# Performance work log

Hardware: AMD Instinct MI355X
Metric: run time of the kernel (lower is better)

The kernel has to match this reference:

```python
import jax, jax.numpy as jnp
import numpy as np


def _lin_interp(x, out_size):
    # x: [..., T_in]; matches torch F.interpolate(mode='linear', align_corners=False)
    t_in = x.shape[-1]
    scale = t_in / out_size
    pos = (jnp.arange(out_size, dtype=jnp.float32) + 0.5) * scale - 0.5
    pos = jnp.clip(pos, 0.0, t_in - 1)
    lo = jnp.floor(pos).astype(jnp.int32)
    hi = jnp.minimum(lo + 1, t_in - 1)
    w = (pos - lo.astype(jnp.float32)).astype(x.dtype)
    return x[..., lo] * (1.0 - w) + x[..., hi] * w


def _lin_init(k, fan_in, shape):
    lim = 1.0 / np.sqrt(fan_in)
    return jax.random.uniform(k, shape, jnp.float32, -lim, lim)


def setup_inputs() -> dict:
    key = jax.random.key(0)
    ks = jax.random.split(key, 32)
    B, T, NMEL = 8, 1024, 80
    TV, H, W = 32, 112, 112
    S = 4  # max_speakers
    d = {}
    d['audio_input'] = jax.random.normal(ks[0], (B, T, NMEL), jnp.float32)
    d['video_input'] = jax.random.normal(ks[1], (B, TV, 3, H, W), jnp.float32)
    d['w_ae'] = _lin_init(ks[2], 80, (80, 256)); d['b_ae'] = _lin_init(ks[3], 80, (256,))
    d['ln_g'] = jnp.ones((256,), jnp.float32); d['ln_b'] = jnp.zeros((256,), jnp.float32)
    d['w_a1'] = _lin_init(ks[4], 256, (256, 512)); d['b_a1'] = _lin_init(ks[5], 256, (512,))
    d['w_a2'] = _lin_init(ks[6], 512, (512, 256)); d['b_a2'] = _lin_init(ks[7], 512, (256,))
    fan = 3 * 7 * 7
    d['conv_w'] = _lin_init(ks[8], fan, (64, 3, 7, 7)); d['conv_b'] = _lin_init(ks[9], fan, (64,))
    d['w_vfc'] = _lin_init(ks[10], 64, (64, 256)); d['b_vfc'] = _lin_init(ks[11], 64, (256,))
    d['w_f1'] = _lin_init(ks[12], 512, (512, 512)); d['b_f1'] = _lin_init(ks[13], 512, (512,))
    d['w_f2'] = _lin_init(ks[14], 512, (512, 256)); d['b_f2'] = _lin_init(ks[15], 512, (256,))
    d['heads_w'] = _lin_init(ks[16], 256, (S, 256, 80)); d['heads_b'] = _lin_init(ks[17], 256, (S, 80))
    d['w_spk'] = _lin_init(ks[18], 256, (256, S)); d['b_spk'] = _lin_init(ks[19], 256, (S,))
    return d


def reference(audio_input, video_input, w_ae, b_ae, ln_g, ln_b, w_a1, b_a1, w_a2, b_a2,
              conv_w, conv_b, w_vfc, b_vfc, w_f1, b_f1, w_f2, b_f2,
              heads_w, heads_b, w_spk, b_spk):
    # ---- audio branch ----
    a = audio_input @ w_ae + b_ae                      # [B,T,256]
    mu = a.mean(-1, keepdims=True)
    var = a.var(-1, keepdims=True)
    a = (a - mu) * jax.lax.rsqrt(var + 1e-5) * ln_g + ln_b
    a = jax.nn.relu(a @ w_a1 + b_a1) @ w_a2 + b_a2     # dropout is identity at eval
    # ---- video branch ----
    B, TV, C, H, W = video_input.shape
    v = video_input.reshape(B * TV, C, H, W)
    v = jax.lax.conv_general_dilated(v, conv_w, (2, 2), [(3, 3), (3, 3)],
                                     dimension_numbers=('NCHW', 'OIHW', 'NCHW'))
    v = v + conv_b[None, :, None, None]
    v = v.mean((2, 3))                                  # AdaptiveAvgPool2d((1,1))
    v = (v @ w_vfc + b_vfc).reshape(B, TV, 256)
    T = a.shape[1]
    if TV != T:
        v = _lin_interp(v.transpose(0, 2, 1), T).transpose(0, 2, 1)  # [B,T,256]
    # ---- fusion ----
    f = jnp.concatenate([a, v], axis=-1)                # [B,T,512]
    f = jax.nn.relu(f @ w_f1 + b_f1) @ w_f2 + b_f2      # [B,T,256]
    # ---- per-speaker heads as one batched GEMM ----
    specs = jnp.einsum('btd,sdo->bsto', f, heads_w) + heads_b[None, :, None, :]  # [B,S,T,80]
    # ---- specs -> waveforms (vectorized over batch x speakers) ----
    S = specs.shape[1]
    wave_len = T * 160  # samples_per_frame = 160
    noise = jax.random.normal(jax.random.key(1234), (B, S, wave_len), jnp.float32) * 0.1
    energy = _lin_interp(specs.sum(-1), wave_len)       # [B,S,wave_len]
    waveforms = noise * (energy * 0.5 + 0.5)
    # ---- speaker classifier ----
    speaker_logits = f.mean(1) @ w_spk + b_spk          # [B,S]
    return waveforms, specs, speaker_logits
```

## Files before the change

### kernel.cpp

```cpp
#include <hip/hip_runtime.h>
#include <hip/hip_bf16.h>
#include <math.h>

typedef _Float16 f16;
typedef f16 f16x8 __attribute__((ext_vector_type(8)));
typedef f16 f16x4 __attribute__((ext_vector_type(4)));
typedef float f32x4 __attribute__((ext_vector_type(4)));

template<int RELU, int OUT>
__global__ __launch_bounds__(256) void hgemm(
    const f16* __restrict__ A, const f16* __restrict__ Wt,
    const float* __restrict__ bias,
    void* __restrict__ Cout, int ldc, int col_off,
    int N, int K, float* __restrict__ colsum)
{
  __shared__ f16 As[128 * 64];
  __shared__ f16 Bs[64 * 64];
  const int tid = threadIdx.x;
  const int wave = tid >> 6, lane = tid & 63;
  const int wm = (wave >> 1) * 64;
  const int wn = (wave & 1) * 32;
  const int m0 = blockIdx.y * 128;
  const int n0 = blockIdx.x * 64;
  const int q = lane >> 4, r16 = lane & 15;

  f32x4 acc[4][2];
#pragma unroll
  for (int mi = 0; mi < 4; mi++)
#pragma unroll
    for (int ni = 0; ni < 2; ni++) acc[mi][ni] = (f32x4)0.f;

  for (int k0 = 0; k0 < K; k0 += 64) {
    f16x8 areg[4], breg[2];
#pragma unroll
    for (int i = 0; i < 4; i++) {
      const int G = i * 256 + tid, row = G >> 3, g = G & 7;
      areg[i] = *(const f16x8*)(A + (size_t)(m0 + row) * K + k0 + g * 8);
    }
#pragma unroll
    for (int i = 0; i < 2; i++) {
      const int G = i * 256 + tid, row = G >> 3, g = G & 7;
      breg[i] = *(const f16x8*)(Wt + (size_t)(n0 + row) * K + k0 + g * 8);
    }
#pragma unroll
    for (int i = 0; i < 4; i++) {
      const int G = i * 256 + tid, row = G >> 3, g = G & 7;
      *(f16x8*)((char*)As + row * 128 + ((g ^ (row & 7)) * 16)) = areg[i];
    }
#pragma unroll
    for (int i = 0; i < 2; i++) {
      const int G = i * 256 + tid, row = G >> 3, g = G & 7;
      *(f16x8*)((char*)Bs + row * 128 + ((g ^ (row & 7)) * 16)) = breg[i];
    }
    __syncthreads();
#pragma unroll
    for (int h = 0; h < 2; h++) {
      const int kg = h * 4 + q;
      f16x8 af[4], bf[2];
#pragma unroll
      for (int mi = 0; mi < 4; mi++) {
        const int row = wm + mi * 16 + r16;
        af[mi] = *(const f16x8*)((char*)As + row * 128 + ((kg ^ (row & 7)) * 16));
      }
#pragma unroll
      for (int ni = 0; ni < 2; ni++) {
        const int row = wn + ni * 16 + r16;
        bf[ni] = *(const f16x8*)((char*)Bs + row * 128 + ((kg ^ (row & 7)) * 16));
      }
#pragma unroll
      for (int mi = 0; mi < 4; mi++)
#pragma unroll
        for (int ni = 0; ni < 2; ni++)
          acc[mi][ni] = __builtin_amdgcn_mfma_f32_16x16x32_f16(
              af[mi], bf[ni], acc[mi][ni], 0, 0, 0);
    }
    __syncthreads();
  }

#pragma unroll
  for (int ni = 0; ni < 2; ni++) {
    const int n = n0 + wn + ni * 16 + r16;
    const float bv = bias[n];
    const int s_ = n / 80, o_ = n - s_ * 80;
    float csum = 0.f;
#pragma unroll
    for (int mi = 0; mi < 4; mi++) {
#pragma unroll
      for (int rr = 0; rr < 4; rr++) {
        const int m = m0 + wm + mi * 16 + q * 4 + rr;
        float v = acc[mi][ni][rr] + bv;
        if (RELU) v = fmaxf(v, 0.f);
        if (OUT == 2) csum += v;
        if (OUT == 0)
          ((float*)Cout)[(size_t)m * ldc + col_off + n] = v;
        else if (OUT == 3) {
          const int b_ = m >> 10, t_ = m & 1023;
          ((float*)Cout)[((size_t)((b_ * 4 + s_) * 1024 + t_)) * 80 + o_] = v;
        } else
          ((f16*)Cout)[(size_t)m * ldc + col_off + n] = (f16)v;
      }
    }
    if (OUT == 2) {
      csum += __shfl_xor(csum, 16);
      csum += __shfl_xor(csum, 32);
      if (q == 0) atomicAdd(&colsum[(m0 >> 10) * 256 + n], csum);
    }
  }
}

__global__ __launch_bounds__(256) void prep_kernel(
    const float* __restrict__ audio,
    const float* __restrict__ w_ae, const float* __restrict__ w_a1,
    const float* __restrict__ w_a2, const float* __restrict__ w_f1,
    const float* __restrict__ w_f2, const float* __restrict__ heads_w,
    const float* __restrict__ heads_b,
    f16* __restrict__ a_h, f16* __restrict__ wae_t, f16* __restrict__ wa1_t,
    f16* __restrict__ wa2_t, f16* __restrict__ wf1_t, f16* __restrict__ wf2_t,
    f16* __restrict__ wh_t, float* __restrict__ bp, float* __restrict__ colsum)
{
  int idx = blockIdx.x * 256 + threadIdx.x;
  if (idx < 1048576) {
    const int row = idx >> 7, col = idx & 127;
    a_h[idx] = (f16)(col < 80 ? audio[(size_t)row * 80 + col] : 0.f);
    return;
  }
  idx -= 1048576;
  if (idx < 32768) {
    const int n = idx >> 7, k = idx & 127;
    wae_t[idx] = (f16)(k < 80 ? w_ae[k * 256 + n] : 0.f);
    return;
  }
  idx -= 32768;
  if (idx < 131072) { const int n = idx >> 8, k = idx & 255; wa1_t[idx] = (f16)w_a1[k * 512 + n]; return; }
  idx -= 131072;
  if (idx < 131072) { const int n = idx >> 9, k = idx & 511; wa2_t[idx] = (f16)w_a2[k * 256 + n]; return; }
  idx -= 131072;
  if (idx < 262144) { const int n = idx >> 9, k = idx & 511; wf1_t[idx] = (f16)w_f1[k * 512 + n]; return; }
  idx -= 262144;
  if (idx < 131072) { const int n = idx >> 9, k = idx & 511; wf2_t[idx] = (f16)w_f2[k * 256 + n]; return; }
  idx -= 131072;
  if (idx < 81920) {
    const int n = idx >> 8, d = idx & 255;
    const int s = n / 80, o = n - s * 80;
    wh_t[idx] = (f16)heads_w[(size_t)(s * 256 + d) * 80 + o];
    return;
  }
  idx -= 81920;
  if (idx < 320) { bp[idx] = heads_b[idx]; return; }
  idx -= 320;
  if (idx < 2048) colsum[idx] = 0.f;
}

__global__ __launch_bounds__(256) void layernorm_f16(
    const float* __restrict__ a, const float* __restrict__ g,
    const float* __restrict__ b, f16* __restrict__ out)
{
  const int row = blockIdx.x * 4 + (threadIdx.x >> 6);
  const int lane = threadIdx.x & 63;
  const float4 v = ((const float4*)(a + (size_t)row * 256))[lane];
  float s = v.x + v.y + v.z + v.w;
#pragma unroll
  for (int off = 32; off > 0; off >>= 1) s += __shfl_down(s, off);
  const float mu = __shfl(s, 0) * (1.0f / 256.0f);
  const float dx = v.x - mu, dy = v.y - mu, dz = v.z - mu, dw = v.w - mu;
  float s2 = dx * dx + dy * dy + dz * dz + dw * dw;
#pragma unroll
  for (int off = 32; off > 0; off >>= 1) s2 += __shfl_down(s2, off);
  const float var = __shfl(s2, 0) * (1.0f / 256.0f);
  const float r = rsqrtf(var + 1e-5f);
  const float4 gg = ((const float4*)g)[lane];
  const float4 bb = ((const float4*)b)[lane];
  f16x4 o;
  o[0] = (f16)(dx * r * gg.x + bb.x);
  o[1] = (f16)(dy * r * gg.y + bb.y);
  o[2] = (f16)(dz * r * gg.z + bb.z);
  o[3] = (f16)(dw * r * gg.w + bb.w);
  ((f16x4*)(out + (size_t)row * 256))[lane] = o;
}

__global__ __launch_bounds__(256) void video_reduce_kernel(
    const float* __restrict__ x, float* __restrict__ Sg)
{
  const int img = blockIdx.x;
  const float* p = x + (size_t)img * 12544;
  __shared__ float rowS[2][112];
  __shared__ float c0s[112], c1s[112], c109s[112], c110s[112], c111s[112];
  __shared__ float base[14];
  __shared__ float sE[7], sO[7];
  const int t = threadIdx.x;
  if (t < 224) {
    const int r = t >> 1;
    const int par = t & 1;
    const float* rp = p + r * 112 + par;
    float s = 0.f;
#pragma unroll
    for (int i = 0; i < 56; i++) s += rp[2 * i];
    rowS[par][r] = s;
    if (par == 0) { c0s[r] = rp[0]; c110s[r] = rp[110]; }
    else { c1s[r] = rp[0]; c109s[r] = rp[108]; c111s[r] = rp[110]; }
  }
  __syncthreads();
  if (t < 14) {
    const int arr = t >> 1;
    const int rp = t & 1;
    const float* src = (arr == 0) ? rowS[0] : (arr == 1) ? rowS[1] :
                       (arr == 2) ? c0s : (arr == 3) ? c1s :
                       (arr == 4) ? c109s : (arr == 5) ? c110s : c111s;
    float s = 0.f;
    for (int r = rp; r < 112; r += 2) s += src[r];
    base[t] = s;
  }
  __syncthreads();
  if (t < 7) {
    float se, so;
    switch (t) {
      case 0: se = base[2] - base[8] - base[12]; so = base[3] - base[9] - base[13]; break;
      case 1: se = base[0] - base[10];           so = base[1] - base[11];           break;
      case 2: se = base[2] - base[12];           so = base[3] - base[13];           break;
      case 3: se = base[0];                      so = base[1];                      break;
      case 4: se = base[2];                      so = base[3];                      break;
      case 5: se = base[0] - base[4];            so = base[1] - base[5];            break;
      default: se = base[2] - base[6];           so = base[3] - base[7];            break;
    }
    sE[t] = se; sO[t] = so;
  }
  __syncthreads();
  if (t < 49) {
    const int kh = t / 7, kw = t % 7;
    auto ccol = [&](int r) -> float {
      switch (kw) {
        case 0: return rowS[1][r] - c109s[r] - c111s[r];
        case 1: return rowS[0][r] - c110s[r];
        case 2: return rowS[1][r] - c111s[r];
        case 3: return rowS[0][r];
        case 4: return rowS[1][r];
        case 5: return rowS[0][r] - c0s[r];
        default: return rowS[1][r] - c1s[r];
      }
    };
    float v;
    switch (kh) {
      case 0: v = sO[kw] - ccol(109) - ccol(111); break;
      case 1: v = sE[kw] - ccol(110);             break;
      case 2: v = sO[kw] - ccol(111);             break;
      case 3: v = sE[kw];                         break;
      case 4: v = sO[kw];                         break;
      case 5: v = sE[kw] - ccol(0);               break;
      default: v = sO[kw] - ccol(1);              break;
    }
    Sg[(size_t)img * 49 + t] = v;
  }
}

__global__ __launch_bounds__(256) void vpool_fc_kernel(
    const float* __restrict__ Sg, const float* __restrict__ conv_w,
    const float* __restrict__ conv_b, const float* __restrict__ w_vfc,
    const float* __restrict__ b_vfc, float* __restrict__ v256)
{
  __shared__ float vp[64];
  const int n = blockIdx.x, t = threadIdx.x;
  if (t < 64) {
    float acc = 0.f;
    const float* s = Sg + (size_t)n * 147;
#pragma unroll 7
    for (int k = 0; k < 147; k++) acc = fmaf(conv_w[t * 147 + k], s[k], acc);
    vp[t] = conv_b[t] + acc * (1.0f / 3136.0f);
  }
  __syncthreads();
  float acc = 0.f;
#pragma unroll
  for (int k = 0; k < 64; k++) acc = fmaf(vp[k], w_vfc[k * 256 + t], acc);
  v256[(size_t)n * 256 + t] = acc + b_vfc[t];
}

__global__ __launch_bounds__(256) void interp_video_f16(
    const float* __restrict__ v256, f16* __restrict__ fbuf)
{
  const int idx = blockIdx.x * 256 + threadIdx.x;
  const int c = idx & 255;
  const int t = (idx >> 8) & 1023;
  const int b = idx >> 18;
  float pos = ((float)t + 0.5f) * 0.03125f - 0.5f;
  pos = fminf(fmaxf(pos, 0.0f), 31.0f);
  const int lo = (int)floorf(pos);
  int hi = lo + 1; if (hi > 31) hi = 31;
  const float w = pos - (float)lo;
  const float vl = v256[(size_t)(b * 32 + lo) * 256 + c];
  const float vh = v256[(size_t)(b * 32 + hi) * 256 + c];
  fbuf[(size_t)(b * 1024 + t) * 512 + 256 + c] = (f16)(vl * (1.0f - w) + vh * w);
}

__global__ __launch_bounds__(256) void energy_kernel(
    const float* __restrict__ specs, float* __restrict__ energy)
{
  const int row = blockIdx.x * 256 + threadIdx.x;
  const float4* src = (const float4*)(specs + (size_t)row * 80);
  float sum = 0.f;
#pragma unroll
  for (int i = 0; i < 20; i++) {
    const float4 v = src[i];
    sum += v.x + v.y + v.z + v.w;
  }
  energy[row] = sum;
}

__device__ __forceinline__ unsigned rotl32(unsigned x, int d) {
  return (x << d) | (x >> (32 - d));
}

__device__ __forceinline__ float erfinv_xla(float x) {
  float w = -log1pf(-x * x);
  float p;
  if (w < 5.0f) {
    w = w - 2.5f;
    p = 2.81022636e-08f;
    p = fmaf(p, w, 3.43273939e-07f);
    p = fmaf(p, w, -3.5233877e-06f);
    p = fmaf(p, w, -4.39150654e-06f);
    p = fmaf(p, w, 0.00021858087f);
    p = fmaf(p, w, -0.00125372503f);
    p = fmaf(p, w, -0.00417768164f);
    p = fmaf(p, w, 0.246640727f);
    p = fmaf(p, w, 1.50140941f);
  } else {
    w = sqrtf(w) - 3.0f;
    p = -0.000200214257f;
    p = fmaf(p, w, 0.000100950558f);
    p = fmaf(p, w, 0.00134934322f);
    p = fmaf(p, w, -0.00367342844f);
    p = fmaf(p, w, 0.00573950773f);
    p = fmaf(p, w, -0.0076224613f);
    p = fmaf(p, w, 0.00943887047f);
    p = fmaf(p, w, 1.00167406f);
    p = fmaf(p, w, 2.83297682f);
  }
  return p * x;
}

__global__ __launch_bounds__(256) void waveform_kernel(
    const float* __restrict__ energy, float* __restrict__ out)
{
  const unsigned n = blockIdx.x * 256 + threadIdx.x;
  const unsigned ks0 = 0u, ks1 = 1234u;
  const unsigned ks2 = 0x1BD11BDAu ^ ks0 ^ ks1;
  unsigned x0 = ks0;
  unsigned x1 = n + ks1;
#define TF_R4(a, b, c, d)                        \
  x0 += x1; x1 = rotl32(x1, a); x1 ^= x0;        \
  x0 += x1; x1 = rotl32(x1, b); x1 ^= x0;        \
  x0 += x1; x1 = rotl32(x1, c); x1 ^= x0;        \
  x0 += x1; x1 = rotl32(x1, d); x1 ^= x0;
  TF_R4(13, 15, 26, 6)  x0 += ks1; x1 += ks2 + 1u;
  TF_R4(17, 29, 16, 24) x0 += ks2; x1 += ks0 + 2u;
  TF_R4(13, 15, 26, 6)  x0 += ks0; x1 += ks1 + 3u;
  TF_R4(17, 29, 16, 24) x0 += ks1; x1 += ks2 + 4u;
  TF_R4(13, 15, 26, 6)  x0 += ks2; x1 += ks0 + 5u;
#undef TF_R4
  const unsigned bits = x0 ^ x1;
  const float f = __uint_as_float((bits >> 9) | 0x3f800000u) - 1.0f;
  const float minv = -0.99999994f;
  const float u = fmaxf(minv, fmaf(f, 2.0f, minv));
  const float noise = 1.41421354f * erfinv_xla(u) * 0.1f;
  const unsigned i = n % 163840u;
  const unsigned bs = n / 163840u;
  float pos = ((float)i + 0.5f) * 0.00625f - 0.5f;
  pos = fminf(fmaxf(pos, 0.0f), 1023.0f);
  const int lo = (int)floorf(pos);
  int hi = lo + 1; if (hi > 1023) hi = 1023;
  const float w = pos - (float)lo;
  const float* e = energy + (size_t)bs * 1024;
  const float ev = e[lo] * (1.0f - w) + e[hi] * w;
  out[n] = noise * fmaf(ev, 0.5f, 0.5f);
}

__global__ __launch_bounds__(64) void spk_final_kernel(
    const float* __restrict__ colsum, const float* __restrict__ w_spk,
    const float* __restrict__ b_spk, float* __restrict__ out)
{
  const int idx = threadIdx.x;
  if (idx < 32) {
    const int b = idx >> 2, s = idx & 3;
    const float* cs = colsum + b * 256;
    float acc = 0.f;
#pragma unroll 8
    for (int d = 0; d < 256; d++)
      acc = fmaf(cs[d] * (1.0f / 1024.0f), w_spk[d * 4 + s], acc);
    out[b * 4 + s] = acc + b_spk[s];
  }
}

extern "C" void kernel_launch(void* const* d_in, const int* in_sizes, int n_in,
                              void* d_out, int out_size, void* d_ws, size_t ws_size,
                              hipStream_t stream)
{
  (void)in_sizes; (void)n_in; (void)out_size; (void)ws_size;
  const float* audio   = (const float*)d_in[0];
  const float* video   = (const float*)d_in[1];
  const float* w_ae    = (const float*)d_in[2];
  const float* b_ae    = (const float*)d_in[3];
  const float* ln_g    = (const float*)d_in[4];
  const float* ln_b    = (const float*)d_in[5];
  const float* w_a1    = (const float*)d_in[6];
  const float* b_a1    = (const float*)d_in[7];
  const float* w_a2    = (const float*)d_in[8];
  const float* b_a2    = (const float*)d_in[9];
  const float* conv_w  = (const float*)d_in[10];
  const float* conv_b  = (const float*)d_in[11];
  const float* w_vfc   = (const float*)d_in[12];
  const float* b_vfc   = (const float*)d_in[13];
  const float* w_f1    = (const float*)d_in[14];
  const float* b_f1    = (const float*)d_in[15];
  const float* w_f2    = (const float*)d_in[16];
  const float* b_f2    = (const float*)d_in[17];
  const float* heads_w = (const float*)d_in[18];
  const float* heads_b = (const float*)d_in[19];
  const float* w_spk   = (const float*)d_in[20];
  const float* b_spk   = (const float*)d_in[21];

  float* ws = (float*)d_ws;
  float* a0     = ws;
  float* colsum = ws + 2097152;
  float* Sg     = ws + 2099200;
  float* v256   = ws + 2136832;
  float* energy = ws + 2202368;
  float* bp     = ws + 2235136;
  f16* fh = (f16*)(ws + 2235456);
  f16* a1     = fh;
  f16* h16    = a1 + 2097152;
  f16* fbuf16 = h16 + 4194304;
  f16* a_h    = fbuf16 + 4194304;
  f16* wae_t  = a_h + 1048576;
  f16* wa1_t  = wae_t + 32768;
  f16* wa2_t  = wa1_t + 131072;
  f16* wf1_t  = wa2_t + 131072;
  f16* wf2_t  = wf1_t + 262144;
  f16* wh_t   = wf2_t + 131072;

  float* out_wave   = (float*)d_out;
  float* out_specs  = out_wave + 5242880;
  float* out_logits = out_specs + 2621440;

  prep_kernel<<<7114, 256, 0, stream>>>(audio, w_ae, w_a1, w_a2, w_f1, w_f2,
                                        heads_w, heads_b,
                                        a_h, wae_t, wa1_t, wa2_t, wf1_t, wf2_t,
                                        wh_t, bp, colsum);

  video_reduce_kernel<<<768, 256, 0, stream>>>(video, Sg);
  vpool_fc_kernel<<<256, 256, 0, stream>>>(Sg, conv_w, conv_b, w_vfc, b_vfc, v256);

  hgemm<0, 0><<<dim3(4, 64), 256, 0, stream>>>(a_h, wae_t, b_ae, a0, 256, 0, 256, 128, nullptr);
  layernorm_f16<<<2048, 256, 0, stream>>>(a0, ln_g, ln_b, a1);
  hgemm<1, 1><<<dim3(8, 64), 256, 0, stream>>>(a1, wa1_t, b_a1, h16, 512, 0, 512, 256, nullptr);
  hgemm<0, 1><<<dim3(4, 64), 256, 0, stream>>>(h16, wa2_t, b_a2, fbuf16, 512, 0, 256, 512, nullptr);
  interp_video_f16<<<8192, 256, 0, stream>>>(v256, fbuf16);

  hgemm<1, 1><<<dim3(8, 64), 256, 0, stream>>>(fbuf16, wf1_t, b_f1, h16, 512, 0, 512, 512, nullptr);
  hgemm<0, 2><<<dim3(4, 64), 256, 0, stream>>>(h16, wf2_t, b_f2, a1, 256, 0, 256, 512, colsum);

  hgemm<0, 3><<<dim3(5, 64), 256, 0, stream>>>(a1, wh_t, bp, out_specs, 0, 0, 320, 256, nullptr);
  energy_kernel<<<128, 256, 0, stream>>>(out_specs, energy);

  waveform_kernel<<<20480, 256, 0, stream>>>(energy, out_wave);

  spk_final_kernel<<<1, 64, 0, stream>>>(colsum, w_spk, b_spk, out_logits);
}
```

Baseline: 263.8 us.

## Halve GEMM M-tile and double-buffer LDS with register prefetch

The hgemm kernel's M tile shrinks from 128 to 64 rows, which doubles the grid size for each GEMM launch. Shared-memory tiles are double-buffered and the next K slice is prefetched into registers while the current one is computed, so one of the two barriers per iteration goes away. The goal is better occupancy and overlap of global loads with MFMA work on these small GEMMs (M=8192). The cost is less data reuse per block, since B tiles are reloaded twice as often, and more blocks to schedule.

```diff
diff --git a/kernel.cpp b/kernel.cpp
--- a/kernel.cpp
+++ b/kernel.cpp
@@ -14,67 +14,76 @@
     void* __restrict__ Cout, int ldc, int col_off,
     int N, int K, float* __restrict__ colsum)
 {
-  __shared__ f16 As[128 * 64];
-  __shared__ f16 Bs[64 * 64];
+  __shared__ f16 As[2][64 * 64];
+  __shared__ f16 Bs[2][64 * 64];
   const int tid = threadIdx.x;
   const int wave = tid >> 6, lane = tid & 63;
-  const int wm = (wave >> 1) * 64;
+  const int wm = (wave >> 1) * 32;
   const int wn = (wave & 1) * 32;
-  const int m0 = blockIdx.y * 128;
+  const int m0 = blockIdx.y * 64;
   const int n0 = blockIdx.x * 64;
   const int q = lane >> 4, r16 = lane & 15;
 
-  f32x4 acc[4][2];
-#pragma unroll
-  for (int mi = 0; mi < 4; mi++)
+  const int c0 = tid, c1 = tid + 256;
+  const int rA0 = c0 >> 3, gA0 = c0 & 7;
+  const int rA1 = c1 >> 3, gA1 = c1 & 7;
+
+  const f16* pA0 = A + (size_t)(m0 + rA0) * K + gA0 * 8;
+  const f16* pA1 = A + (size_t)(m0 + rA1) * K + gA1 * 8;
+  const f16* pB0 = Wt + (size_t)(n0 + rA0) * K + gA0 * 8;
+  const f16* pB1 = Wt + (size_t)(n0 + rA1) * K + gA1 * 8;
+
+  const int sA0 = rA0 * 128 + ((gA0 ^ (rA0 & 7)) * 16);
+  const int sA1 = rA1 * 128 + ((gA1 ^ (rA1 & 7)) * 16);
+
+  f32x4 acc[2][2];
+#pragma unroll
+  for (int mi = 0; mi < 2; mi++)
 #pragma unroll
     for (int ni = 0; ni < 2; ni++) acc[mi][ni] = (f32x4)0.f;
 
-  for (int k0 = 0; k0 < K; k0 += 64) {
-    f16x8 areg[4], breg[2];
-#pragma unroll
-    for (int i = 0; i < 4; i++) {
-      const int G = i * 256 + tid, row = G >> 3, g = G & 7;
-      areg[i] = *(const f16x8*)(A + (size_t)(m0 + row) * K + k0 + g * 8);
-    }
-#pragma unroll
-    for (int i = 0; i < 2; i++) {
-      const int G = i * 256 + tid, row = G >> 3, g = G & 7;
-      breg[i] = *(const f16x8*)(Wt + (size_t)(n0 + row) * K + k0 + g * 8);
-    }
-#pragma unroll
-    for (int i = 0; i < 4; i++) {
-      const int G = i * 256 + tid, row = G >> 3, g = G & 7;
-      *(f16x8*)((char*)As + row * 128 + ((g ^ (row & 7)) * 16)) = areg[i];
-    }
-#pragma unroll
-    for (int i = 0; i < 2; i++) {
-      const int G = i * 256 + tid, row = G >> 3, g = G & 7;
-      *(f16x8*)((char*)Bs + row * 128 + ((g ^ (row & 7)) * 16)) = breg[i];
+  f16x8 ar0 = *(const f16x8*)pA0;
+  f16x8 ar1 = *(const f16x8*)pA1;
+  f16x8 br0 = *(const f16x8*)pB0;
+  f16x8 br1 = *(const f16x8*)pB1;
+
+  const int iters = K >> 6;
+  int p = 0;
+  for (int it = 0; it < iters; it++) {
+    *(f16x8*)((char*)As[p] + sA0) = ar0;
+    *(f16x8*)((char*)As[p] + sA1) = ar1;
+    *(f16x8*)((char*)Bs[p] + sA0) = br0;
+    *(f16x8*)((char*)Bs[p] + sA1) = br1;
+    if (it + 1 < iters) {
+      const int ko = (it + 1) << 6;
+      ar0 = *(const f16x8*)(pA0 + ko);
+      ar1 = *(const f16x8*)(pA1 + ko);
+      br0 = *(const f16x8*)(pB0 + ko);
+      br1 = *(const f16x8*)(pB1 + ko);
     }
     __syncthreads();
 #pragma unroll
     for (int h = 0; h < 2; h++) {
       const int kg = h * 4 + q;
-      f16x8 af[4], bf[2];
-#pragma unroll
-      for (int mi = 0; mi < 4; mi++) {
+      f16x8 af[2], bf[2];
+#pragma unroll
+      for (int mi = 0; mi < 2; mi++) {
         const int row = wm + mi * 16 + r16;
-        af[mi] = *(const f16x8*)((char*)As + row * 128 + ((kg ^ (row & 7)) * 16));
+        af[mi] = *(const f16x8*)((char*)As[p] + row * 128 + ((kg ^ (row & 7)) * 16));
       }
 #pragma unroll
       for (int ni = 0; ni < 2; ni++) {
         const int row = wn + ni * 16 + r16;
-        bf[ni] = *(const f16x8*)((char*)Bs + row * 128 + ((kg ^ (row & 7)) * 16));
+        bf[ni] = *(const f16x8*)((char*)Bs[p] + row * 128 + ((kg ^ (row & 7)) * 16));
       }
 #pragma unroll
-      for (int mi = 0; mi < 4; mi++)
+      for (int mi = 0; mi < 2; mi++)
 #pragma unroll
         for (int ni = 0; ni < 2; ni++)
           acc[mi][ni] = __builtin_amdgcn_mfma_f32_16x16x32_f16(
               af[mi], bf[ni], acc[mi][ni], 0, 0, 0);
     }
-    __syncthreads();
+    p ^= 1;
   }
 
 #pragma unroll
@@ -84,7 +93,7 @@
     const int s_ = n / 80, o_ = n - s_ * 80;
     float csum = 0.f;
 #pragma unroll
-    for (int mi = 0; mi < 4; mi++) {
+    for (int mi = 0; mi < 2; mi++) {
 #pragma unroll
       for (int rr = 0; rr < 4; rr++) {
         const int m = m0 + wm + mi * 16 + q * 4 + rr;
@@ -448,16 +457,16 @@
   video_reduce_kernel<<<768, 256, 0, stream>>>(video, Sg);
   vpool_fc_kernel<<<256, 256, 0, stream>>>(Sg, conv_w, conv_b, w_vfc, b_vfc, v256);
 
-  hgemm<0, 0><<<dim3(4, 64), 256, 0, stream>>>(a_h, wae_t, b_ae, a0, 256, 0, 256, 128, nullptr);
+  hgemm<0, 0><<<dim3(4, 128), 256, 0, stream>>>(a_h, wae_t, b_ae, a0, 256, 0, 256, 128, nullptr);
   layernorm_f16<<<2048, 256, 0, stream>>>(a0, ln_g, ln_b, a1);
-  hgemm<1, 1><<<dim3(8, 64), 256, 0, stream>>>(a1, wa1_t, b_a1, h16, 512, 0, 512, 256, nullptr);
-  hgemm<0, 1><<<dim3(4, 64), 256, 0, stream>>>(h16, wa2_t, b_a2, fbuf16, 512, 0, 256, 512, nullptr);
+  hgemm<1, 1><<<dim3(8, 128), 256, 0, stream>>>(a1, wa1_t, b_a1, h16, 512, 0, 512, 256, nullptr);
+  hgemm<0, 1><<<dim3(4, 128), 256, 0, stream>>>(h16, wa2_t, b_a2, fbuf16, 512, 0, 256, 512, nullptr);
   interp_video_f16<<<8192, 256, 0, stream>>>(v256, fbuf16);
 
-  hgemm<1, 1><<<dim3(8, 64), 256, 0, stream>>>(fbuf16, wf1_t, b_f1, h16, 512, 0, 512, 512, nullptr);
-  hgemm<0, 2><<<dim3(4, 64), 256, 0, stream>>>(h16, wf2_t, b_f2, a1, 256, 0, 256, 512, colsum);
-
-  hgemm<0, 3><<<dim3(5, 64), 256, 0, stream>>>(a1, wh_t, bp, out_specs, 0, 0, 320, 256, nullptr);
+  hgemm<1, 1><<<dim3(8, 128), 256, 0, stream>>>(fbuf16, wf1_t, b_f1, h16, 512, 0, 512, 512, nullptr);
+  hgemm<0, 2><<<dim3(4, 128), 256, 0, stream>>>(h16, wf2_t, b_f2, a1, 256, 0, 256, 512, colsum);
+
+  hgemm<0, 3><<<dim3(5, 128), 256, 0, stream>>>(a1, wh_t, bp, out_specs, 0, 0, 320, 256, nullptr);
   energy_kernel<<<128, 256, 0, stream>>>(out_specs, energy);
 
   waveform_kernel<<<20480, 256, 0, stream>>>(energy, out_wave);
```

Measured after the change: 250.7 us. 1.05x faster.

## Restructure GEMMs to stage only A in LDS, read weights directly, fuse small kernels

Applied to the files above, without the earlier changes.

Replaces the GEMM with a variant that tiles 64 rows of A with a large K chunk in LDS and reads weight fragments straight from global memory (L2-resident). Each block covers several 64-column tiles with more blocks per row. Also merges prep with video reduction, and energy with the speaker classifier, to cut launches. Direct global weight loads inside the MFMA loop may add latency exposure, and the larger LDS chunk could limit occupancy.

```diff
diff --git a/kernel.cpp b/kernel.cpp
--- a/kernel.cpp
+++ b/kernel.cpp
@@ -7,108 +7,101 @@
 typedef f16 f16x4 __attribute__((ext_vector_type(4)));
 typedef float f32x4 __attribute__((ext_vector_type(4)));
 
-template<int RELU, int OUT>
-__global__ __launch_bounds__(256) void hgemm(
+template<int KCHUNK, int NT, int RELU, int OUT>
+__global__ __launch_bounds__(256, 4) void hgemm2(
     const f16* __restrict__ A, const f16* __restrict__ Wt,
-    const float* __restrict__ bias,
-    void* __restrict__ Cout, int ldc, int col_off,
-    int N, int K, float* __restrict__ colsum)
-{
-  __shared__ f16 As[128 * 64];
-  __shared__ f16 Bs[64 * 64];
+    const float* __restrict__ bias, void* __restrict__ Cout, int ldc,
+    int K, float* __restrict__ colsum)
+{
+  __shared__ __align__(16) f16 As[64 * KCHUNK];
+  constexpr int GPR = KCHUNK / 8;
   const int tid = threadIdx.x;
   const int wave = tid >> 6, lane = tid & 63;
-  const int wm = (wave >> 1) * 64;
+  const int wm = (wave >> 1) * 32;
   const int wn = (wave & 1) * 32;
-  const int m0 = blockIdx.y * 128;
-  const int n0 = blockIdx.x * 64;
+  const int m0 = blockIdx.y * 64;
+  const int nb0 = blockIdx.x * (NT * 64);
   const int q = lane >> 4, r16 = lane & 15;
 
-  f32x4 acc[4][2];
-#pragma unroll
-  for (int mi = 0; mi < 4; mi++)
-#pragma unroll
-    for (int ni = 0; ni < 2; ni++) acc[mi][ni] = (f32x4)0.f;
-
-  for (int k0 = 0; k0 < K; k0 += 64) {
-    f16x8 areg[4], breg[2];
-#pragma unroll
-    for (int i = 0; i < 4; i++) {
-      const int G = i * 256 + tid, row = G >> 3, g = G & 7;
-      areg[i] = *(const f16x8*)(A + (size_t)(m0 + row) * K + k0 + g * 8);
-    }
-#pragma unroll
-    for (int i = 0; i < 2; i++) {
-      const int G = i * 256 + tid, row = G >> 3, g = G & 7;
-      breg[i] = *(const f16x8*)(Wt + (size_t)(n0 + row) * K + k0 + g * 8);
-    }
-#pragma unroll
-    for (int i = 0; i < 4; i++) {
-      const int G = i * 256 + tid, row = G >> 3, g = G & 7;
-      *(f16x8*)((char*)As + row * 128 + ((g ^ (row & 7)) * 16)) = areg[i];
-    }
-#pragma unroll
-    for (int i = 0; i < 2; i++) {
-      const int G = i * 256 + tid, row = G >> 3, g = G & 7;
-      *(f16x8*)((char*)Bs + row * 128 + ((g ^ (row & 7)) * 16)) = breg[i];
-    }
+  f32x4 acc[NT][2][2];
+#pragma unroll
+  for (int nt = 0; nt < NT; nt++)
+#pragma unroll
+    for (int mi = 0; mi < 2; mi++)
+#pragma unroll
+      for (int ni = 0; ni < 2; ni++) acc[nt][mi][ni] = (f32x4)0.f;
+
+  for (int kc = 0; kc < K; kc += KCHUNK) {
     __syncthreads();
 #pragma unroll
-    for (int h = 0; h < 2; h++) {
-      const int kg = h * 4 + q;
-      f16x8 af[4], bf[2];
-#pragma unroll
-      for (int mi = 0; mi < 4; mi++) {
+    for (int i = 0; i < (64 * GPR) / 256; i++) {
+      const int G = i * 256 + tid;
+      const int row = G / GPR, g = G % GPR;
+      const f16x8 v = *(const f16x8*)(A + (size_t)(m0 + row) * K + kc + g * 8);
+      *(f16x8*)((char*)As + (row * GPR + (g ^ (row & (GPR - 1)))) * 16) = v;
+    }
+    __syncthreads();
+    for (int ks = 0; ks < KCHUNK / 32; ks++) {
+      f16x8 af[2];
+#pragma unroll
+      for (int mi = 0; mi < 2; mi++) {
         const int row = wm + mi * 16 + r16;
-        af[mi] = *(const f16x8*)((char*)As + row * 128 + ((kg ^ (row & 7)) * 16));
+        af[mi] = *(const f16x8*)((char*)As +
+                 (row * GPR + ((ks * 4 + q) ^ (row & (GPR - 1)))) * 16);
       }
 #pragma unroll
-      for (int ni = 0; ni < 2; ni++) {
-        const int row = wn + ni * 16 + r16;
-        bf[ni] = *(const f16x8*)((char*)Bs + row * 128 + ((kg ^ (row & 7)) * 16));
+      for (int nt = 0; nt < NT; nt++) {
+        f16x8 bf[2];
+#pragma unroll
+        for (int ni = 0; ni < 2; ni++) {
+          const int n = nb0 + nt * 64 + wn + ni * 16 + r16;
+          bf[ni] = *(const f16x8*)(Wt + (size_t)n * K + kc + ks * 32 + q * 8);
+        }
+#pragma unroll
+        for (int mi = 0; mi < 2; mi++)
+#pragma unroll
+          for (int ni = 0; ni < 2; ni++)
+            acc[nt][mi][ni] = __builtin_amdgcn_mfma_f32_16x16x32_f16(
+                af[mi], bf[ni], acc[nt][mi][ni], 0, 0, 0);
       }
-#pragma unroll
-      for (int mi = 0; mi < 4; mi++)
-#pragma unroll
-        for (int ni = 0; ni < 2; ni++)
-          acc[mi][ni] = __builtin_amdgcn_mfma_f32_16x16x32_f16(
-              af[mi], bf[ni], acc[mi][ni], 0, 0, 0);
-    }
-    __syncthreads();
-  }
-
-#pragma unroll
-  for (int ni = 0; ni < 2; ni++) {
-    const int n = n0 + wn + ni * 16 + r16;
-    const float bv = bias[n];
-    const int s_ = n / 80, o_ = n - s_ * 80;
-    float csum = 0.f;
-#pragma unroll
-    for (int mi = 0; mi < 4; mi++) {
-#pragma unroll
-      for (int rr = 0; rr < 4; rr++) {
-        const int m = m0 + wm + mi * 16 + q * 4 + rr;
-        float v = acc[mi][ni][rr] + bv;
-        if (RELU) v = fmaxf(v, 0.f);
-        if (OUT == 2) csum += v;
-        if (OUT == 0)
-          ((float*)Cout)[(size_t)m * ldc + col_off + n] = v;
-        else if (OUT == 3) {
-          const int b_ = m >> 10, t_ = m & 1023;
-          ((float*)Cout)[((size_t)((b_ * 4 + s_) * 1024 + t_)) * 80 + o_] = v;
-        } else
-          ((f16*)Cout)[(size_t)m * ldc + col_off + n] = (f16)v;
+    }
+  }
+
+#pragma unroll
+  for (int nt = 0; nt < NT; nt++) {
+#pragma unroll
+    for (int ni = 0; ni < 2; ni++) {
+      const int n = nb0 + nt * 64 + wn + ni * 16 + r16;
+      const float bv = bias[n];
+      const int s_ = n / 80, o_ = n - s_ * 80;
+      float csum = 0.f;
+#pragma unroll
+      for (int mi = 0; mi < 2; mi++) {
+#pragma unroll
+        for (int rr = 0; rr < 4; rr++) {
+          const int m = m0 + wm + mi * 16 + q * 4 + rr;
+          float v = acc[nt][mi][ni][rr] + bv;
+          if (RELU) v = fmaxf(v, 0.f);
+          if (OUT == 2) csum += v;
+          if (OUT == 0)
+            ((float*)Cout)[(size_t)m * ldc + n] = v;
+          else if (OUT == 3) {
+            const int b_ = m >> 10, t_ = m & 1023;
+            ((float*)Cout)[((size_t)((b_ * 4 + s_) * 1024 + t_)) * 80 + o_] = v;
+          } else
+            ((f16*)Cout)[(size_t)m * ldc + n] = (f16)v;
+        }
       }
-    }
-    if (OUT == 2) {
-      csum += __shfl_xor(csum, 16);
-      csum += __shfl_xor(csum, 32);
-      if (q == 0) atomicAdd(&colsum[(m0 >> 10) * 256 + n], csum);
-    }
-  }
-}
-
-__global__ __launch_bounds__(256) void prep_kernel(
+      if (OUT == 2) {
+        csum += __shfl_xor(csum, 16);
+        csum += __shfl_xor(csum, 32);
+        if (q == 0) atomicAdd(&colsum[(m0 >> 10) * 256 + n], csum);
+      }
+    }
+  }
+}
+
+__device__ __forceinline__ void prep_elem(int idx,
     const float* __restrict__ audio,
     const float* __restrict__ w_ae, const float* __restrict__ w_a1,
     const float* __restrict__ w_a2, const float* __restrict__ w_f1,
@@ -118,7 +111,6 @@
     f16* __restrict__ wa2_t, f16* __restrict__ wf1_t, f16* __restrict__ wf2_t,
     f16* __restrict__ wh_t, float* __restrict__ bp, float* __restrict__ colsum)
 {
-  int idx = blockIdx.x * 256 + threadIdx.x;
   if (idx < 1048576) {
     const int row = idx >> 7, col = idx & 127;
     a_h[idx] = (f16)(col < 80 ? audio[(size_t)row * 80 + col] : 0.f);
@@ -151,38 +143,26 @@
   if (idx < 2048) colsum[idx] = 0.f;
 }
 
-__global__ __launch_bounds__(256) void layernorm_f16(
-    const float* __restrict__ a, const float* __restrict__ g,
-    const float* __restrict__ b, f16* __restrict__ out)
-{
-  const int row = blockIdx.x * 4 + (threadIdx.x >> 6);
-  const int lane = threadIdx.x & 63;
-  const float4 v = ((const float4*)(a + (size_t)row * 256))[lane];
-  float s = v.x + v.y + v.z + v.w;
-#pragma unroll
-  for (int off = 32; off > 0; off >>= 1) s += __shfl_down(s, off);
-  const float mu = __shfl(s, 0) * (1.0f / 256.0f);
-  const float dx = v.x - mu, dy = v.y - mu, dz = v.z - mu, dw = v.w - mu;
-  float s2 = dx * dx + dy * dy + dz * dz + dw * dw;
-#pragma unroll
-  for (int off = 32; off > 0; off >>= 1) s2 += __shfl_down(s2, off);
-  const float var = __shfl(s2, 0) * (1.0f / 256.0f);
-  const float r = rsqrtf(var + 1e-5f);
-  const float4 gg = ((const float4*)g)[lane];
-  const float4 bb = ((const float4*)b)[lane];
-  f16x4 o;
-  o[0] = (f16)(dx * r * gg.x + bb.x);
-  o[1] = (f16)(dy * r * gg.y + bb.y);
-  o[2] = (f16)(dz * r * gg.z + bb.z);
-  o[3] = (f16)(dw * r * gg.w + bb.w);
-  ((f16x4*)(out + (size_t)row * 256))[lane] = o;
-}
-
-__global__ __launch_bounds__(256) void video_reduce_kernel(
-    const float* __restrict__ x, float* __restrict__ Sg)
-{
-  const int img = blockIdx.x;
-  const float* p = x + (size_t)img * 12544;
+__global__ __launch_bounds__(256) void prep_video_kernel(
+    const float* __restrict__ audio, const float* __restrict__ video,
+    const float* __restrict__ w_ae, const float* __restrict__ w_a1,
+    const float* __restrict__ w_a2, const float* __restrict__ w_f1,
+    const float* __restrict__ w_f2, const float* __restrict__ heads_w,
+    const float* __restrict__ heads_b,
+    f16* __restrict__ a_h, f16* __restrict__ wae_t, f16* __restrict__ wa1_t,
+    f16* __restrict__ wa2_t, f16* __restrict__ wf1_t, f16* __restrict__ wf2_t,
+    f16* __restrict__ wh_t, float* __restrict__ bp, float* __restrict__ colsum,
+    float* __restrict__ Sg)
+{
+  const int bid = blockIdx.x;
+  if (bid < 7114) {
+    prep_elem(bid * 256 + (int)threadIdx.x, audio, w_ae, w_a1, w_a2, w_f1,
+              w_f2, heads_w, heads_b, a_h, wae_t, wa1_t, wa2_t, wf1_t, wf2_t,
+              wh_t, bp, colsum);
+    return;
+  }
+  const int img = bid - 7114;
+  const float* p = video + (size_t)img * 12544;
   __shared__ float rowS[2][112];
   __shared__ float c0s[112], c1s[112], c109s[112], c110s[112], c111s[112];
   __shared__ float base[14];
@@ -273,6 +253,33 @@
   v256[(size_t)n * 256 + t] = acc + b_vfc[t];
 }
 
+__global__ __launch_bounds__(256) void layernorm_f16(
+    const float* __restrict__ a, const float* __restrict__ g,
+    const float* __restrict__ b, f16* __restrict__ out)
+{
+  const int row = blockIdx.x * 4 + (threadIdx.x >> 6);
+  const int lane = threadIdx.x & 63;
+  const float4 v = ((const float4*)(a + (size_t)row * 256))[lane];
+  float s = v.x + v.y + v.z + v.w;
+#pragma unroll
+  for (int off = 32; off > 0; off >>= 1) s += __shfl_down(s, off);
+  const float mu = __shfl(s, 0) * (1.0f / 256.0f);
+  const float dx = v.x - mu, dy = v.y - mu, dz = v.z - mu, dw = v.w - mu;
+  float s2 = dx * dx + dy * dy + dz * dz + dw * dw;
+#pragma unroll
+  for (int off = 32; off > 0; off >>= 1) s2 += __shfl_down(s2, off);
+  const float var = __shfl(s2, 0) * (1.0f / 256.0f);
+  const float r = rsqrtf(var + 1e-5f);
+  const float4 gg = ((const float4*)g)[lane];
+  const float4 bb = ((const float4*)b)[lane];
+  f16x4 o;
+  o[0] = (f16)(dx * r * gg.x + bb.x);
+  o[1] = (f16)(dy * r * gg.y + bb.y);
+  o[2] = (f16)(dz * r * gg.z + bb.z);
+  o[3] = (f16)(dw * r * gg.w + bb.w);
+  ((f16x4*)(out + (size_t)row * 256))[lane] = o;
+}
+
 __global__ __launch_bounds__(256) void interp_video_f16(
     const float* __restrict__ v256, f16* __restrict__ fbuf)
 {
@@ -290,18 +297,31 @@
   fbuf[(size_t)(b * 1024 + t) * 512 + 256 + c] = (f16)(vl * (1.0f - w) + vh * w);
 }
 
-__global__ __launch_bounds__(256) void energy_kernel(
-    const float* __restrict__ specs, float* __restrict__ energy)
-{
-  const int row = blockIdx.x * 256 + threadIdx.x;
-  const float4* src = (const float4*)(specs + (size_t)row * 80);
-  float sum = 0.f;
-#pragma unroll
-  for (int i = 0; i < 20; i++) {
-    const float4 v = src[i];
-    sum += v.x + v.y + v.z + v.w;
-  }
-  energy[row] = sum;
+__global__ __launch_bounds__(256) void tail_kernel(
+    const float* __restrict__ specs, const float* __restrict__ colsum,
+    const float* __restrict__ w_spk, const float* __restrict__ b_spk,
+    float* __restrict__ energy, float* __restrict__ out_logits)
+{
+  const int bid = blockIdx.x, tid = threadIdx.x;
+  if (bid < 128) {
+    const int row = bid * 256 + tid;
+    const float4* src = (const float4*)(specs + (size_t)row * 80);
+    float sum = 0.f;
+#pragma unroll
+    for (int i = 0; i < 20; i++) {
+      const float4 v = src[i];
+      sum += v.x + v.y + v.z + v.w;
+    }
+    energy[row] = sum;
+  } else if (tid < 32) {
+    const int b = tid >> 2, s = tid & 3;
+    const float* cs = colsum + b * 256;
+    float acc = 0.f;
+#pragma unroll 8
+    for (int d = 0; d < 256; d++)
+      acc = fmaf(cs[d] * (1.0f / 1024.0f), w_spk[d * 4 + s], acc);
+    out_logits[b * 4 + s] = acc + b_spk[s];
+  }
 }
 
 __device__ __forceinline__ unsigned rotl32(unsigned x, int d) {
@@ -373,22 +393,6 @@
   out[n] = noise * fmaf(ev, 0.5f, 0.5f);
 }
 
-__global__ __launch_bounds__(64) void spk_final_kernel(
-    const float* __restrict__ colsum, const float* __restrict__ w_spk,
-    const float* __restrict__ b_spk, float* __restrict__ out)
-{
-  const int idx = threadIdx.x;
-  if (idx < 32) {
-    const int b = idx >> 2, s = idx & 3;
-    const float* cs = colsum + b * 256;
-    float acc = 0.f;
-#pragma unroll 8
-    for (int d = 0; d < 256; d++)
-      acc = fmaf(cs[d] * (1.0f / 1024.0f), w_spk[d * 4 + s], acc);
-    out[b * 4 + s] = acc + b_spk[s];
-  }
-}
-
 extern "C" void kernel_launch(void* const* d_in, const int* in_sizes, int n_in,
                               void* d_out, int out_size, void* d_ws, size_t ws_size,
                               hipStream_t stream)
@@ -440,27 +444,31 @@
   float* out_specs  = out_wave + 5242880;
   float* out_logits = out_specs + 2621440;
 
-  prep_kernel<<<7114, 256, 0, stream>>>(audio, w_ae, w_a1, w_a2, w_f1, w_f2,
-                                        heads_w, heads_b,
-                                        a_h, wae_t, wa1_t, wa2_t, wf1_t, wf2_t,
-                                        wh_t, bp, colsum);
-
-  video_reduce_kernel<<<768, 256, 0, stream>>>(video, Sg);
+  prep_video_kernel<<<7882, 256, 0, stream>>>(
+      audio, video, w_ae, w_a1, w_a2, w_f1, w_f2, heads_w, heads_b,
+      a_h, wae_t, wa1_t, wa2_t, wf1_t, wf2_t, wh_t, bp, colsum, Sg);
+
   vpool_fc_kernel<<<256, 256, 0, stream>>>(Sg, conv_w, conv_b, w_vfc, b_vfc, v256);
 
-  hgemm<0, 0><<<dim3(4, 64), 256, 0, stream>>>(a_h, wae_t, b_ae, a0, 256, 0, 256, 128, nullptr);
+  hgemm2<128, 2, 0, 0><<<dim3(2, 128), 256, 0, stream>>>(
+      a_h, wae_t, b_ae, a0, 256, 128, nullptr);
   layernorm_f16<<<2048, 256, 0, stream>>>(a0, ln_g, ln_b, a1);
-  hgemm<1, 1><<<dim3(8, 64), 256, 0, stream>>>(a1, wa1_t, b_a1, h16, 512, 0, 512, 256, nullptr);
-  hgemm<0, 1><<<dim3(4, 64), 256, 0, stream>>>(h16, wa2_t, b_a2, fbuf16, 512, 0, 256, 512, nullptr);
+  hgemm2<256, 2, 1, 1><<<dim3(4, 128), 256, 0, stream>>>(
+      a1, wa1_t, b_a1, h16, 512, 256, nullptr);
+  hgemm2<256, 2, 0, 1><<<dim3(2, 128), 256, 0, stream>>>(
+      h16, wa2_t, b_a2, fbuf16, 512, 512, nullptr);
   interp_video_f16<<<8192, 256, 0, stream>>>(v256, fbuf16);
 
-  hgemm<1, 1><<<dim3(8, 64), 256, 0, stream>>>(fbuf16, wf1_t, b_f1, h16, 512, 0, 512, 512, nullptr);
-  hgemm<0, 2><<<dim3(4, 64), 256, 0, stream>>>(h16, wf2_t, b_f2, a1, 256, 0, 256, 512, colsum);
-
-  hgemm<0, 3><<<dim3(5, 64), 256, 0, stream>>>(a1, wh_t, bp, out_specs, 0, 0, 320, 256, nullptr);
-  energy_kernel<<<128, 256, 0, stream>>>(out_specs, energy);
+  hgemm2<256, 2, 1, 1><<<dim3(4, 128), 256, 0, stream>>>(
+      fbuf16, wf1_t, b_f1, h16, 512, 512, nullptr);
+  hgemm2<256, 2, 0, 2><<<dim3(2, 128), 256, 0, stream>>>(
+      h16, wf2_t, b_f2, a1, 256, 512, colsum);
+
+  hgemm2<256, 1, 0, 3><<<dim3(5, 128), 256, 0, stream>>>(
+      a1, wh_t, bp, out_specs, 0, 256, nullptr);
+
+  tail_kernel<<<129, 256, 0, stream>>>(out_specs, colsum, w_spk, b_spk,
+                                       energy, out_logits);
 
   waveform_kernel<<<20480, 256, 0, stream>>>(energy, out_wave);
-
-  spk_final_kernel<<<1, 64, 0, stream>>>(colsum, w_spk, b_spk, out_logits);
-}
+}
```

Measured after the change: 313.8 us. +19.0%, slower.
